# Optimization experiments

Hardware: AMD Instinct MI355X
Metric: run time of the kernel (lower is better)

## Reference

```python
import jax, jax.numpy as jnp
import numpy as np

B, T, C, H = 4, 4096, 1024, 128

def setup_inputs() -> dict:
    key = jax.random.key(0)
    k1, k2, k3, k4 = jax.random.split(key, 4)
    x = jax.random.normal(k1, (B, T, C), dtype=jnp.float32)
    # nn.Linear(embed, head, bias=False): y = x @ W, store W as [C, H]
    s = 1.0 / np.sqrt(C)
    Wk = jax.random.normal(k2, (C, H), dtype=jnp.float32) * s
    Wq = jax.random.normal(k3, (C, H), dtype=jnp.float32) * s
    Wv = jax.random.normal(k4, (C, H), dtype=jnp.float32) * s
    return {"x": x, "Wk": Wk, "Wq": Wq, "Wv": Wv}

def reference(x, Wk, Wq, Wv):
    Bx, Tx, Cx = x.shape
    scale = Wk.shape[1] ** -0.5
    k = x @ Wk  # [B,T,H]
    q = x @ Wq
    v = x @ Wv
    att = jnp.einsum('bth,bsh->bts', q, k) * scale  # [B,T,T]
    causal = jnp.triu(jnp.ones((Tx, Tx), dtype=bool), k=1)
    att = jnp.where(causal, -jnp.inf, att)
    att = jax.nn.softmax(att, axis=-1)
    # dropout is identity in eval mode
    out = jnp.einsum('bts,bsh->bth', att, v)  # [B,T,H]
    return out
```

## Files before the change

kernel.cpp:

```cpp
#include <hip/hip_runtime.h>
#include <stdint.h>
#include <math.h>

#define B_ 4
#define T_ 4096
#define C_ 1024
#define H_ 128

typedef __attribute__((ext_vector_type(8))) short s16x8;
typedef __attribute__((ext_vector_type(4))) float f32x4;

__device__ __forceinline__ unsigned short f2bf(float f) {
    union { float f; unsigned u; } v; v.f = f;
    unsigned r = v.u + 0x7fffu + ((v.u >> 16) & 1u);
    return (unsigned short)(r >> 16);
}

__device__ __forceinline__ float bf2f(unsigned short s) {
    union { unsigned u; float f; } v; v.u = (unsigned)s << 16; return v.f;
}

__device__ __forceinline__ s16x8 as_frag(uint4 u) {
    union { uint4 u; s16x8 s; } v; v.u = u; return v.s;
}

__host__ __device__ constexpr int chunks128(int CH) {
    int H2 = CH / 2;
    int k = 32 / H2, r = 32 % H2;
    return H2 * k * (k + 1) / 2 + r * (k + 1);
}

#define QSC (0.0883883476f * 1.4426950408f)

__global__ __launch_bounds__(256) void k_wt(const float* __restrict__ Wk,
                                            const float* __restrict__ Wq,
                                            const float* __restrict__ Wv,
                                            unsigned short* __restrict__ Wt) {
    __shared__ float tile[64][65];
    int w = blockIdx.z;
    const float* W = (w == 0) ? Wk : (w == 1) ? Wq : Wv;
    int c0 = blockIdx.x * 64, h0 = blockIdx.y * 64;
    int tid = threadIdx.x;
#pragma unroll
    for (int k = 0; k < 16; k++) {
        int idx = tid + k * 256;
        int r = idx >> 6, c = idx & 63;
        tile[r][c] = W[(size_t)(c0 + r) * H_ + h0 + c];
    }
    __syncthreads();
#pragma unroll
    for (int k = 0; k < 16; k++) {
        int idx = tid + k * 256;
        int hh = idx >> 6, cc = idx & 63;
        Wt[(size_t)(w * H_ + h0 + hh) * C_ + c0 + cc] = f2bf(tile[cc][hh]);
    }
}

__global__ __launch_bounds__(256, 3) void k_qkv(const float* __restrict__ x,
                                                const unsigned short* __restrict__ Wt,
                                                unsigned short* __restrict__ Qb,
                                                unsigned short* __restrict__ Kb,
                                                unsigned short* __restrict__ Vt) {
    __shared__ unsigned short a_lds[2][64 * 72];
    int tid = threadIdx.x;
    int wv = tid >> 6, lane = tid & 63, quad = lane >> 4, lo = lane & 15;
    int r0 = blockIdx.x * 64;
    int cb = blockIdx.y;
    int nt0 = wv * 3;

    f32x4 acc[3][4];
#pragma unroll
    for (int i = 0; i < 3; i++)
#pragma unroll
        for (int j = 0; j < 4; j++) acc[i][j] = (f32x4){0.f, 0.f, 0.f, 0.f};

    const int row_s = tid >> 2;
    const int seg_s = (tid & 3) * 16;
    size_t xbase = (size_t)(r0 + row_s) * C_ + seg_s;

    const unsigned short* wp[3];
#pragma unroll
    for (int nt = 0; nt < 3; nt++)
        wp[nt] = Wt + (size_t)(cb * 192 + (nt0 + nt) * 16 + lo) * C_ + quad * 8;

    auto pack_store = [&](unsigned short* buf, const float4 (&f)[4]) {
        uint4 u0, u1;
        u0.x = (unsigned)f2bf(f[0].x) | ((unsigned)f2bf(f[0].y) << 16);
        u0.y = (unsigned)f2bf(f[0].z) | ((unsigned)f2bf(f[0].w) << 16);
        u0.z = (unsigned)f2bf(f[1].x) | ((unsigned)f2bf(f[1].y) << 16);
        u0.w = (unsigned)f2bf(f[1].z) | ((unsigned)f2bf(f[1].w) << 16);
        u1.x = (unsigned)f2bf(f[2].x) | ((unsigned)f2bf(f[2].y) << 16);
        u1.y = (unsigned)f2bf(f[2].z) | ((unsigned)f2bf(f[2].w) << 16);
        u1.z = (unsigned)f2bf(f[3].x) | ((unsigned)f2bf(f[3].y) << 16);
        u1.w = (unsigned)f2bf(f[3].z) | ((unsigned)f2bf(f[3].w) << 16);
        *(uint4*)&buf[row_s * 72 + seg_s] = u0;
        *(uint4*)&buf[row_s * 72 + seg_s + 8] = u1;
    };
    auto load_x = [&](float4 (&f)[4], int kc) {
        const float* xp = x + xbase + kc * 64;
#pragma unroll
        for (int j = 0; j < 4; j++) f[j] = *(const float4*)(xp + j * 4);
    };

    float4 xr[4];
    load_x(xr, 0);
    pack_store(a_lds[0], xr);
    __syncthreads();

    for (int kc = 0; kc < 16; kc++) {
        const unsigned short* buf = a_lds[kc & 1];
        float4 xn[4];
        if (kc < 15) load_x(xn, kc + 1);
        s16x8 b[3][2];
#pragma unroll
        for (int nt = 0; nt < 3; nt++)
#pragma unroll
            for (int kh = 0; kh < 2; kh++)
                b[nt][kh] = *(const s16x8*)(wp[nt] + kc * 64 + kh * 32);
        s16x8 af[4][2];
#pragma unroll
        for (int mt = 0; mt < 4; mt++)
#pragma unroll
            for (int kh = 0; kh < 2; kh++)
                af[mt][kh] = *(const s16x8*)&buf[(mt * 16 + lo) * 72 + kh * 32 + quad * 8];
#pragma unroll
        for (int nt = 0; nt < 3; nt++)
#pragma unroll
            for (int kh = 0; kh < 2; kh++)
#pragma unroll
                for (int mt = 0; mt < 4; mt++)
                    acc[nt][mt] = __builtin_amdgcn_mfma_f32_16x16x32_bf16(
                        af[mt][kh], b[nt][kh], acc[nt][mt], 0, 0, 0);
        if (kc < 15) pack_store((unsigned short*)a_lds[(kc & 1) ^ 1], xn);
        __syncthreads();
    }

#pragma unroll
    for (int nt = 0; nt < 3; nt++) {
        int col = cb * 192 + (nt0 + nt) * 16 + lo;
        int w = col >> 7, h = col & 127;
#pragma unroll
        for (int mt = 0; mt < 4; mt++) {
            int mrow = r0 + mt * 16 + quad * 4;
            if (w == 2) {
                int b = mrow >> 12, t0 = mrow & 4095;
                int tp = (t0 & ~31) + (((t0 & 15) >> 2) << 3) + (((t0 >> 4) & 1) << 2);
                uint2 pk;
                pk.x = (unsigned)f2bf(acc[nt][mt][0]) | ((unsigned)f2bf(acc[nt][mt][1]) << 16);
                pk.y = (unsigned)f2bf(acc[nt][mt][2]) | ((unsigned)f2bf(acc[nt][mt][3]) << 16);
                *(uint2*)(Vt + (size_t)(b * H_ + h) * T_ + tp) = pk;
            } else if (w == 1) {
                unsigned short* dst = Qb + (size_t)mrow * H_ + h;
#pragma unroll
                for (int r = 0; r < 4; r++)
                    dst[(size_t)r * H_] = f2bf(acc[nt][mt][r] * QSC);
            } else {
                unsigned short* dst = Kb + (size_t)mrow * H_ + h;
#pragma unroll
                for (int r = 0; r < 4; r++)
                    dst[(size_t)r * H_] = f2bf(acc[nt][mt][r]);
            }
        }
    }
}

#define LOAD_KV(kv0)                                                            \
    do {                                                                        \
        const uint4* kg = (const uint4*)(Kb + (size_t)(batch * T_ + (kv0) + srow_k) * H_); \
        pk0 = kg[sseg_k + 0]; pk1 = kg[sseg_k + 1];                             \
        const uint4* vg = (const uint4*)(Vt + (size_t)(batch * H_ + srow_v) * T_ + (kv0)); \
        pv0 = vg[sseg_v + 0]; pv1 = vg[sseg_v + 1];                             \
    } while (0)

template <int CH>
__global__ __launch_bounds__(512, 4) void k_attn(const unsigned short* __restrict__ Qb,
                                                 const unsigned short* __restrict__ Kb,
                                                 const unsigned short* __restrict__ Vt,
                                                 unsigned short* __restrict__ Opart,
                                                 float* __restrict__ Mpart,
                                                 float* __restrict__ Lpart,
                                                 float* __restrict__ out) {
    __shared__ uint4 kbuf[64 * 16];
    __shared__ uint4 vbuf[128 * 8];

    int tid = threadIdx.x;
    int wv = tid >> 6, lane = tid & 63, quad = lane >> 4, lo = lane & 15;

    int id = blockIdx.x;
    int batch = id & 3;
    int slot = id >> 2;
    int s = slot, q = 31;
    for (;;) { int nc = (2 * q + 1 + CH) / CH; if (s < nc) break; s -= nc; --q; }
    int qb = q;
    int tbeg = s * CH;
    int tend = min(tbeg + CH, 2 * qb + 2);
    int m0 = qb * 128 + wv * 16;
    int query = m0 + lo;

    s16x8 qf[4];
    size_t qrow = (size_t)(batch * T_ + m0 + lo) * H_;
#pragma unroll
    for (int ks = 0; ks < 4; ks++)
        qf[ks] = *(const s16x8*)(Qb + qrow + ks * 32 + quad * 8);

    f32x4 acc_o[8];
#pragma unroll
    for (int o = 0; o < 8; o++) acc_o[o] = (f32x4){0.f, 0.f, 0.f, 0.f};
    float m_i = -INFINITY, l_i = 0.f;

    const int srow_k = tid >> 3, sseg_k = (tid & 7) * 2;
    const int srow_v = tid >> 2, sseg_v = (tid & 3) * 2;

    uint4 pk0, pk1, pv0, pv1;
    LOAD_KV(tbeg * 64);

    for (int t = tbeg; t < tend; ++t) {
        int kv0 = t * 64;
        kbuf[srow_k * 16 + ((sseg_k + 0) ^ (srow_k & 15))] = pk0;
        kbuf[srow_k * 16 + ((sseg_k + 1) ^ (srow_k & 15))] = pk1;
        vbuf[srow_v * 8 + ((sseg_v + 0) ^ (srow_v & 7))] = pv0;
        vbuf[srow_v * 8 + ((sseg_v + 1) ^ (srow_v & 7))] = pv1;
        __syncthreads();
        if (t + 1 < tend) LOAD_KV((t + 1) * 64);

        f32x4 s_acc[4];
#pragma unroll
        for (int nt = 0; nt < 4; nt++) s_acc[nt] = (f32x4){0.f, 0.f, 0.f, 0.f};
        __builtin_amdgcn_s_setprio(1);
#pragma unroll
        for (int ks = 0; ks < 4; ks++) {
#pragma unroll
            for (int nt = 0; nt < 4; nt++) {
                s16x8 kf = as_frag(kbuf[(nt * 16 + lo) * 16 + ((ks * 4 + quad) ^ lo)]);
                s_acc[nt] = __builtin_amdgcn_mfma_f32_16x16x32_bf16(kf, qf[ks], s_acc[nt], 0, 0, 0);
            }
        }
        __builtin_amdgcn_s_setprio(0);

        float p[4][4];
#pragma unroll
        for (int nt = 0; nt < 4; nt++)
#pragma unroll
            for (int r = 0; r < 4; r++) p[nt][r] = s_acc[nt][r];
        if (kv0 + 63 > m0) {
#pragma unroll
            for (int nt = 0; nt < 4; nt++)
#pragma unroll
                for (int r = 0; r < 4; r++)
                    if (kv0 + nt * 16 + quad * 4 + r > query) p[nt][r] = -INFINITY;
        }

        float mx = p[0][0];
#pragma unroll
        for (int nt = 0; nt < 4; nt++)
#pragma unroll
            for (int r = 0; r < 4; r++) mx = fmaxf(mx, p[nt][r]);
        if (__any(mx > m_i + 8.0f)) {
            float rm = fmaxf(mx, __shfl_xor(mx, 16));
            rm = fmaxf(rm, __shfl_xor(rm, 32));
            float mnew = fmaxf(m_i, rm);
            float alpha = exp2f(m_i - mnew);
            l_i *= alpha;
            m_i = mnew;
#pragma unroll
            for (int o = 0; o < 8; o++)
#pragma unroll
                for (int r = 0; r < 4; r++) acc_o[o][r] *= alpha;
        }
        float rs = 0.f;
#pragma unroll
        for (int nt = 0; nt < 4; nt++)
#pragma unroll
            for (int r = 0; r < 4; r++) {
                float pv = exp2f(p[nt][r] - m_i);
                p[nt][r] = pv;
                rs += pv;
            }
        l_i += rs;

        s16x8 pf[2];
#pragma unroll
        for (int kt = 0; kt < 2; kt++) {
            uint4 u;
            u.x = (__float_as_uint(p[2 * kt][0]) >> 16) | ((__float_as_uint(p[2 * kt][1]) >> 16) << 16);
            u.y = (__float_as_uint(p[2 * kt][2]) >> 16) | ((__float_as_uint(p[2 * kt][3]) >> 16) << 16);
            u.z = (__float_as_uint(p[2 * kt + 1][0]) >> 16) | ((__float_as_uint(p[2 * kt + 1][1]) >> 16) << 16);
            u.w = (__float_as_uint(p[2 * kt + 1][2]) >> 16) | ((__float_as_uint(p[2 * kt + 1][3]) >> 16) << 16);
            pf[kt] = as_frag(u);
        }

        __builtin_amdgcn_s_setprio(1);
#pragma unroll
        for (int kt = 0; kt < 2; kt++)
#pragma unroll
            for (int o = 0; o < 8; o++) {
                int vrow = o * 16 + lo;
                s16x8 vf = as_frag(vbuf[vrow * 8 + ((kt * 4 + quad) ^ (vrow & 7))]);
                acc_o[o] = __builtin_amdgcn_mfma_f32_16x16x32_bf16(vf, pf[kt], acc_o[o], 0, 0, 0);
            }
        __builtin_amdgcn_s_setprio(0);
        __syncthreads();
    }

    l_i += __shfl_xor(l_i, 16);
    l_i += __shfl_xor(l_i, 32);

    bool direct = (tbeg == 0) && (tend == 2 * qb + 2);
    if (direct) {
        float inv = 1.0f / l_i;
        int rowg = batch * T_ + m0 + lo;
#pragma unroll
        for (int o = 0; o < 8; o++) {
            float4 v = {acc_o[o][0] * inv, acc_o[o][1] * inv,
                        acc_o[o][2] * inv, acc_o[o][3] * inv};
            *(float4*)(out + (size_t)rowg * H_ + o * 16 + quad * 4) = v;
        }
    } else {
        constexpr int NCH = chunks128(CH);
        size_t pr = (size_t)(batch * NCH + slot) * 128 + wv * 16 + lo;
        unsigned short* Op = Opart + pr * 128;
#pragma unroll
        for (int o = 0; o < 8; o++) {
            uint2 pk;
            pk.x = (unsigned)f2bf(acc_o[o][0]) | ((unsigned)f2bf(acc_o[o][1]) << 16);
            pk.y = (unsigned)f2bf(acc_o[o][2]) | ((unsigned)f2bf(acc_o[o][3]) << 16);
            *(uint2*)(Op + o * 16 + quad * 4) = pk;
        }
        if (quad == 0) { Mpart[pr] = m_i; Lpart[pr] = l_i; }
    }
}

template <int CH>
__global__ __launch_bounds__(256) void k_comb(const unsigned short* __restrict__ Opart,
                                              const float* __restrict__ Mpart,
                                              const float* __restrict__ Lpart,
                                              float* __restrict__ out) {
    constexpr int NCH = chunks128(CH);
    constexpr int H2 = CH / 2;
    int tid = threadIdx.x;
    int row = blockIdx.x * 8 + (tid >> 5);
    int h4 = (tid & 31) * 4;
    int batch = row >> 12, t = row & 4095, qb = t >> 7, rr = t & 127;
    int nc = (2 * qb + 1 + CH) / CH;
    if (nc == 1) return;
    int n = qb + 1, k = n / H2, r = n % H2;
    int F = H2 * k * (k + 1) / 2 + r * (k + 1);
    int base = NCH - F;
    float M = -INFINITY, den = 0.f;
    float4 o = {0.f, 0.f, 0.f, 0.f};
    for (int s = 0; s < nc; ++s) {
        size_t pr = (size_t)(batch * NCH + base + s) * 128 + rr;
        float ms = Mpart[pr], ls = Lpart[pr];
        uint2 u = *(const uint2*)(Opart + pr * 128 + h4);
        float4 v = {bf2f((unsigned short)(u.x & 0xffff)),
                    bf2f((unsigned short)(u.x >> 16)),
                    bf2f((unsigned short)(u.y & 0xffff)),
                    bf2f((unsigned short)(u.y >> 16))};
        float Mn = fmaxf(M, ms);
        float wa = exp2f(M - Mn), wb = exp2f(ms - Mn);
        den = den * wa + ls * wb;
        o.x = o.x * wa + v.x * wb;
        o.y = o.y * wa + v.y * wb;
        o.z = o.z * wa + v.z * wb;
        o.w = o.w * wa + v.w * wb;
        M = Mn;
    }
    float inv = 1.0f / den;
    float4 rz = {o.x * inv, o.y * inv, o.z * inv, o.w * inv};
    *(float4*)(out + (size_t)row * H_ + h4) = rz;
}

extern "C" void kernel_launch(void* const* d_in, const int* in_sizes, int n_in,
                              void* d_out, int out_size, void* d_ws, size_t ws_size,
                              hipStream_t stream) {
    const float* x  = (const float*)d_in[0];
    const float* Wk = (const float*)d_in[1];
    const float* Wq = (const float*)d_in[2];
    const float* Wv = (const float*)d_in[3];
    char* ws = (char*)d_ws;
    unsigned short* Wt = (unsigned short*)ws;
    unsigned short* Qb = (unsigned short*)(ws + (1u << 20));
    unsigned short* Kb = (unsigned short*)(ws + (5u << 20));
    unsigned short* Vt = (unsigned short*)(ws + (9u << 20));
    float* out = (float*)d_out;

    const size_t base = (size_t)13 << 20;
    constexpr int N8  = chunks128(8);
    constexpr int N16 = chunks128(16);
    auto need_for = [&](int nch) {
        return base + (size_t)4 * nch * 128 * (128 * 2) + 2 * (size_t)4 * nch * 128 * 4;
    };

    k_wt  <<<dim3(16, 2, 3), 256, 0, stream>>>(Wk, Wq, Wv, Wt);
    k_qkv <<<dim3(256, 2), 256, 0, stream>>>(x, Wt, Qb, Kb, Vt);

    if (ws_size >= need_for(N8)) {
        unsigned short* Op = (unsigned short*)(ws + base);
        float* Mp = (float*)(ws + base + (size_t)4 * N8 * 128 * 256);
        float* Lp = Mp + (size_t)4 * N8 * 128;
        k_attn<8><<<4 * N8, 512, 0, stream>>>(Qb, Kb, Vt, Op, Mp, Lp, out);
        k_comb<8><<<2048, 256, 0, stream>>>(Op, Mp, Lp, out);
    } else {
        unsigned short* Op = (unsigned short*)(ws + base);
        float* Mp = (float*)(ws + base + (size_t)4 * N16 * 128 * 256);
        float* Lp = Mp + (size_t)4 * N16 * 128;
        k_attn<16><<<4 * N16, 512, 0, stream>>>(Qb, Kb, Vt, Op, Mp, Lp, out);
        k_comb<16><<<2048, 256, 0, stream>>>(Op, Mp, Lp, out);
    }
}
```

Baseline: 166.7 us.

## Double-buffer K/V shared tiles and enlarge split-KV chunk size

Makes the K and V shared-memory tiles double-buffered. The next tile is written to the alternate buffer after the PV MMAs, and the global load runs two tiles ahead. This removes one barrier per iteration and lets the LDS writes overlap compute. It also raises the split-KV chunk size from 8 to 10 tiles (16 to 20 in the fallback), which means fewer partial blocks and less combine work but coarser load balance. Shared memory per block doubles to 64KB, which may limit how many blocks fit per CU.

```diff
diff --git a/kernel.cpp b/kernel.cpp
--- a/kernel.cpp
+++ b/kernel.cpp
@@ -172,6 +172,14 @@
         pv0 = vg[sseg_v + 0]; pv1 = vg[sseg_v + 1];                             \
     } while (0)
 
+#define STAGE_KV(kw, vw)                                                        \
+    do {                                                                        \
+        (kw)[srow_k * 16 + ((sseg_k + 0) ^ (srow_k & 15))] = pk0;               \
+        (kw)[srow_k * 16 + ((sseg_k + 1) ^ (srow_k & 15))] = pk1;               \
+        (vw)[srow_v * 8 + ((sseg_v + 0) ^ (srow_v & 7))] = pv0;                 \
+        (vw)[srow_v * 8 + ((sseg_v + 1) ^ (srow_v & 7))] = pv1;                 \
+    } while (0)
+
 template <int CH>
 __global__ __launch_bounds__(512, 4) void k_attn(const unsigned short* __restrict__ Qb,
                                                  const unsigned short* __restrict__ Kb,
@@ -180,8 +188,8 @@
                                                  float* __restrict__ Mpart,
                                                  float* __restrict__ Lpart,
                                                  float* __restrict__ out) {
-    __shared__ uint4 kbuf[64 * 16];
-    __shared__ uint4 vbuf[128 * 8];
+    __shared__ uint4 kbuf[2][64 * 16];
+    __shared__ uint4 vbuf[2][128 * 8];
 
     int tid = threadIdx.x;
     int wv = tid >> 6, lane = tid & 63, quad = lane >> 4, lo = lane & 15;
@@ -213,15 +221,15 @@
 
     uint4 pk0, pk1, pv0, pv1;
     LOAD_KV(tbeg * 64);
+    STAGE_KV(kbuf[0], vbuf[0]);
+    if (tbeg + 1 < tend) LOAD_KV((tbeg + 1) * 64);
+    __syncthreads();
 
     for (int t = tbeg; t < tend; ++t) {
+        int cur = (t - tbeg) & 1;
+        const uint4* kb = kbuf[cur];
+        const uint4* vb = vbuf[cur];
         int kv0 = t * 64;
-        kbuf[srow_k * 16 + ((sseg_k + 0) ^ (srow_k & 15))] = pk0;
-        kbuf[srow_k * 16 + ((sseg_k + 1) ^ (srow_k & 15))] = pk1;
-        vbuf[srow_v * 8 + ((sseg_v + 0) ^ (srow_v & 7))] = pv0;
-        vbuf[srow_v * 8 + ((sseg_v + 1) ^ (srow_v & 7))] = pv1;
-        __syncthreads();
-        if (t + 1 < tend) LOAD_KV((t + 1) * 64);
 
         f32x4 s_acc[4];
 #pragma unroll
@@ -231,7 +239,7 @@
         for (int ks = 0; ks < 4; ks++) {
 #pragma unroll
             for (int nt = 0; nt < 4; nt++) {
-                s16x8 kf = as_frag(kbuf[(nt * 16 + lo) * 16 + ((ks * 4 + quad) ^ lo)]);
+                s16x8 kf = as_frag(kb[(nt * 16 + lo) * 16 + ((ks * 4 + quad) ^ lo)]);
                 s_acc[nt] = __builtin_amdgcn_mfma_f32_16x16x32_bf16(kf, qf[ks], s_acc[nt], 0, 0, 0);
             }
         }
@@ -295,10 +303,15 @@
 #pragma unroll
             for (int o = 0; o < 8; o++) {
                 int vrow = o * 16 + lo;
-                s16x8 vf = as_frag(vbuf[vrow * 8 + ((kt * 4 + quad) ^ (vrow & 7))]);
+                s16x8 vf = as_frag(vb[vrow * 8 + ((kt * 4 + quad) ^ (vrow & 7))]);
                 acc_o[o] = __builtin_amdgcn_mfma_f32_16x16x32_bf16(vf, pf[kt], acc_o[o], 0, 0, 0);
             }
         __builtin_amdgcn_s_setprio(0);
+
+        if (t + 1 < tend) {
+            STAGE_KV(kbuf[cur ^ 1], vbuf[cur ^ 1]);
+            if (t + 2 < tend) LOAD_KV((t + 2) * 64);
+        }
         __syncthreads();
     }
 
@@ -385,8 +398,8 @@
     float* out = (float*)d_out;
 
     const size_t base = (size_t)13 << 20;
-    constexpr int N8  = chunks128(8);
-    constexpr int N16 = chunks128(16);
+    constexpr int N10 = chunks128(10);
+    constexpr int N20 = chunks128(20);
     auto need_for = [&](int nch) {
         return base + (size_t)4 * nch * 128 * (128 * 2) + 2 * (size_t)4 * nch * 128 * 4;
     };
@@ -394,17 +407,17 @@
     k_wt  <<<dim3(16, 2, 3), 256, 0, stream>>>(Wk, Wq, Wv, Wt);
     k_qkv <<<dim3(256, 2), 256, 0, stream>>>(x, Wt, Qb, Kb, Vt);
 
-    if (ws_size >= need_for(N8)) {
+    if (ws_size >= need_for(N10)) {
         unsigned short* Op = (unsigned short*)(ws + base);
-        float* Mp = (float*)(ws + base + (size_t)4 * N8 * 128 * 256);
-        float* Lp = Mp + (size_t)4 * N8 * 128;
-        k_attn<8><<<4 * N8, 512, 0, stream>>>(Qb, Kb, Vt, Op, Mp, Lp, out);
-        k_comb<8><<<2048, 256, 0, stream>>>(Op, Mp, Lp, out);
+        float* Mp = (float*)(ws + base + (size_t)4 * N10 * 128 * 256);
+        float* Lp = Mp + (size_t)4 * N10 * 128;
+        k_attn<10><<<4 * N10, 512, 0, stream>>>(Qb, Kb, Vt, Op, Mp, Lp, out);
+        k_comb<10><<<2048, 256, 0, stream>>>(Op, Mp, Lp, out);
     } else {
         unsigned short* Op = (unsigned short*)(ws + base);
-        float* Mp = (float*)(ws + base + (size_t)4 * N16 * 128 * 256);
-        float* Lp = Mp + (size_t)4 * N16 * 128;
-        k_attn<16><<<4 * N16, 512, 0, stream>>>(Qb, Kb, Vt, Op, Mp, Lp, out);
-        k_comb<16><<<2048, 256, 0, stream>>>(Op, Mp, Lp, out);
-    }
-}
+        float* Mp = (float*)(ws + base + (size_t)4 * N20 * 128 * 256);
+        float* Lp = Mp + (size_t)4 * N20 * 128;
+        k_attn<20><<<4 * N20, 512, 0, stream>>>(Qb, Kb, Vt, Op, Mp, Lp, out);
+        k_comb<20><<<2048, 256, 0, stream>>>(Op, Mp, Lp, out);
+    }
+}
```

After: 162.4 us. 2.6% less time.

## Fuse split-KV combine into attention kernel via last-block atomic counter

Applied to the files above, without the earlier changes.

Removes the separate combine kernel launch. Each split block writes its partial output and max/sum stats, then increments a per-(batch, query-block) atomic counter. The block that arrives last merges all partials for that query block and writes the final output. The split chunk size also changes from 8/16 to 10/20, and a memset resets the counters. This saves one kernel launch and its tail effects, at the cost of a fence, an atomic, a serial combine tail inside the last block, and a memset.

```diff
diff --git a/kernel.cpp b/kernel.cpp
--- a/kernel.cpp
+++ b/kernel.cpp
@@ -172,6 +172,18 @@
         pv0 = vg[sseg_v + 0]; pv1 = vg[sseg_v + 1];                             \
     } while (0)
 
+#define ACC8(u, b)                                                              \
+    do {                                                                        \
+        o[(b) + 0] = o[(b) + 0] * wa + bf2f((unsigned short)((u).x & 0xffff)) * wb; \
+        o[(b) + 1] = o[(b) + 1] * wa + bf2f((unsigned short)((u).x >> 16)) * wb;    \
+        o[(b) + 2] = o[(b) + 2] * wa + bf2f((unsigned short)((u).y & 0xffff)) * wb; \
+        o[(b) + 3] = o[(b) + 3] * wa + bf2f((unsigned short)((u).y >> 16)) * wb;    \
+        o[(b) + 4] = o[(b) + 4] * wa + bf2f((unsigned short)((u).z & 0xffff)) * wb; \
+        o[(b) + 5] = o[(b) + 5] * wa + bf2f((unsigned short)((u).z >> 16)) * wb;    \
+        o[(b) + 6] = o[(b) + 6] * wa + bf2f((unsigned short)((u).w & 0xffff)) * wb; \
+        o[(b) + 7] = o[(b) + 7] * wa + bf2f((unsigned short)((u).w >> 16)) * wb;    \
+    } while (0)
+
 template <int CH>
 __global__ __launch_bounds__(512, 4) void k_attn(const unsigned short* __restrict__ Qb,
                                                  const unsigned short* __restrict__ Kb,
@@ -179,9 +191,11 @@
                                                  unsigned short* __restrict__ Opart,
                                                  float* __restrict__ Mpart,
                                                  float* __restrict__ Lpart,
+                                                 int* __restrict__ cnt,
                                                  float* __restrict__ out) {
     __shared__ uint4 kbuf[64 * 16];
     __shared__ uint4 vbuf[128 * 8];
+    __shared__ int lastf;
 
     int tid = threadIdx.x;
     int wv = tid >> 6, lane = tid & 63, quad = lane >> 4, lo = lane & 15;
@@ -315,59 +329,61 @@
                         acc_o[o][2] * inv, acc_o[o][3] * inv};
             *(float4*)(out + (size_t)rowg * H_ + o * 16 + quad * 4) = v;
         }
-    } else {
-        constexpr int NCH = chunks128(CH);
-        size_t pr = (size_t)(batch * NCH + slot) * 128 + wv * 16 + lo;
-        unsigned short* Op = Opart + pr * 128;
-#pragma unroll
-        for (int o = 0; o < 8; o++) {
-            uint2 pk;
-            pk.x = (unsigned)f2bf(acc_o[o][0]) | ((unsigned)f2bf(acc_o[o][1]) << 16);
-            pk.y = (unsigned)f2bf(acc_o[o][2]) | ((unsigned)f2bf(acc_o[o][3]) << 16);
-            *(uint2*)(Op + o * 16 + quad * 4) = pk;
-        }
-        if (quad == 0) { Mpart[pr] = m_i; Lpart[pr] = l_i; }
-    }
-}
-
-template <int CH>
-__global__ __launch_bounds__(256) void k_comb(const unsigned short* __restrict__ Opart,
-                                              const float* __restrict__ Mpart,
-                                              const float* __restrict__ Lpart,
-                                              float* __restrict__ out) {
+        return;
+    }
+
     constexpr int NCH = chunks128(CH);
     constexpr int H2 = CH / 2;
-    int tid = threadIdx.x;
-    int row = blockIdx.x * 8 + (tid >> 5);
-    int h4 = (tid & 31) * 4;
-    int batch = row >> 12, t = row & 4095, qb = t >> 7, rr = t & 127;
+    size_t pr = (size_t)(batch * NCH + slot) * 128 + wv * 16 + lo;
+    unsigned short* Op = Opart + pr * 128;
+#pragma unroll
+    for (int o = 0; o < 8; o++) {
+        uint2 pk;
+        pk.x = (unsigned)f2bf(acc_o[o][0]) | ((unsigned)f2bf(acc_o[o][1]) << 16);
+        pk.y = (unsigned)f2bf(acc_o[o][2]) | ((unsigned)f2bf(acc_o[o][3]) << 16);
+        *(uint2*)(Op + o * 16 + quad * 4) = pk;
+    }
+    if (quad == 0) { Mpart[pr] = m_i; Lpart[pr] = l_i; }
+
     int nc = (2 * qb + 1 + CH) / CH;
-    if (nc == 1) return;
-    int n = qb + 1, k = n / H2, r = n % H2;
-    int F = H2 * k * (k + 1) / 2 + r * (k + 1);
-    int base = NCH - F;
-    float M = -INFINITY, den = 0.f;
-    float4 o = {0.f, 0.f, 0.f, 0.f};
-    for (int s = 0; s < nc; ++s) {
-        size_t pr = (size_t)(batch * NCH + base + s) * 128 + rr;
-        float ms = Mpart[pr], ls = Lpart[pr];
-        uint2 u = *(const uint2*)(Opart + pr * 128 + h4);
-        float4 v = {bf2f((unsigned short)(u.x & 0xffff)),
-                    bf2f((unsigned short)(u.x >> 16)),
-                    bf2f((unsigned short)(u.y & 0xffff)),
-                    bf2f((unsigned short)(u.y >> 16))};
-        float Mn = fmaxf(M, ms);
-        float wa = exp2f(M - Mn), wb = exp2f(ms - Mn);
-        den = den * wa + ls * wb;
-        o.x = o.x * wa + v.x * wb;
-        o.y = o.y * wa + v.y * wb;
-        o.z = o.z * wa + v.z * wb;
-        o.w = o.w * wa + v.w * wb;
-        M = Mn;
-    }
-    float inv = 1.0f / den;
-    float4 rz = {o.x * inv, o.y * inv, o.z * inv, o.w * inv};
-    *(float4*)(out + (size_t)row * H_ + h4) = rz;
+    __threadfence();
+    if (tid == 0) {
+        int old = atomicAdd(&cnt[batch * 32 + qb], 1);
+        lastf = (old == nc - 1);
+    }
+    __syncthreads();
+    if (!lastf) return;
+    __threadfence();
+
+    {
+        int n = qb + 1, kk = n / H2, rm2 = n % H2;
+        int F = H2 * kk * (kk + 1) / 2 + rm2 * (kk + 1);
+        int cbase = NCH - F;
+        int rr = tid >> 2, cg = (tid & 3) * 32;
+        float M = -INFINITY, den = 0.f;
+        float o[32];
+#pragma unroll
+        for (int i = 0; i < 32; i++) o[i] = 0.f;
+        for (int s2 = 0; s2 < nc; ++s2) {
+            size_t pr2 = (size_t)(batch * NCH + cbase + s2) * 128 + rr;
+            float ms = Mpart[pr2], ls = Lpart[pr2];
+            const uint4* op = (const uint4*)(Opart + pr2 * 128 + cg);
+            uint4 u0 = op[0], u1 = op[1], u2 = op[2], u3 = op[3];
+            float Mn = fmaxf(M, ms);
+            float wa = exp2f(M - Mn), wb = exp2f(ms - Mn);
+            den = den * wa + ls * wb;
+            ACC8(u0, 0); ACC8(u1, 8); ACC8(u2, 16); ACC8(u3, 24);
+            M = Mn;
+        }
+        float inv = 1.0f / den;
+        float* dst = out + (size_t)(batch * T_ + qb * 128 + rr) * H_ + cg;
+#pragma unroll
+        for (int i = 0; i < 8; i++) {
+            float4 v = {o[4 * i + 0] * inv, o[4 * i + 1] * inv,
+                        o[4 * i + 2] * inv, o[4 * i + 3] * inv};
+            *(float4*)(dst + 4 * i) = v;
+        }
+    }
 }
 
 extern "C" void kernel_launch(void* const* d_in, const int* in_sizes, int n_in,
@@ -385,26 +401,28 @@
     float* out = (float*)d_out;
 
     const size_t base = (size_t)13 << 20;
-    constexpr int N8  = chunks128(8);
-    constexpr int N16 = chunks128(16);
+    constexpr int N10 = chunks128(10);
+    constexpr int N20 = chunks128(20);
     auto need_for = [&](int nch) {
-        return base + (size_t)4 * nch * 128 * (128 * 2) + 2 * (size_t)4 * nch * 128 * 4;
+        return base + (size_t)4 * nch * 128 * (128 * 2) + 2 * (size_t)4 * nch * 128 * 4 + 512;
     };
 
     k_wt  <<<dim3(16, 2, 3), 256, 0, stream>>>(Wk, Wq, Wv, Wt);
     k_qkv <<<dim3(256, 2), 256, 0, stream>>>(x, Wt, Qb, Kb, Vt);
 
-    if (ws_size >= need_for(N8)) {
+    if (ws_size >= need_for(N10)) {
         unsigned short* Op = (unsigned short*)(ws + base);
-        float* Mp = (float*)(ws + base + (size_t)4 * N8 * 128 * 256);
-        float* Lp = Mp + (size_t)4 * N8 * 128;
-        k_attn<8><<<4 * N8, 512, 0, stream>>>(Qb, Kb, Vt, Op, Mp, Lp, out);
-        k_comb<8><<<2048, 256, 0, stream>>>(Op, Mp, Lp, out);
+        float* Mp = (float*)(ws + base + (size_t)4 * N10 * 128 * 256);
+        float* Lp = Mp + (size_t)4 * N10 * 128;
+        int* cnt = (int*)(Lp + (size_t)4 * N10 * 128);
+        hipMemsetAsync(cnt, 0, 4 * 32 * sizeof(int), stream);
+        k_attn<10><<<4 * N10, 512, 0, stream>>>(Qb, Kb, Vt, Op, Mp, Lp, cnt, out);
     } else {
         unsigned short* Op = (unsigned short*)(ws + base);
-        float* Mp = (float*)(ws + base + (size_t)4 * N16 * 128 * 256);
-        float* Lp = Mp + (size_t)4 * N16 * 128;
-        k_attn<16><<<4 * N16, 512, 0, stream>>>(Qb, Kb, Vt, Op, Mp, Lp, out);
-        k_comb<16><<<2048, 256, 0, stream>>>(Op, Mp, Lp, out);
-    }
-}
+        float* Mp = (float*)(ws + base + (size_t)4 * N20 * 128 * 256);
+        float* Lp = Mp + (size_t)4 * N20 * 128;
+        int* cnt = (int*)(Lp + (size_t)4 * N20 * 128);
+        hipMemsetAsync(cnt, 0, 4 * 32 * sizeof(int), stream);
+        k_attn<20><<<4 * N20, 512, 0, stream>>>(Qb, Kb, Vt, Op, Mp, Lp, cnt, out);
+    }
+}
```

Result: slower. 311.6 us (+87.0%).
